# Kernel optimization log

Hardware: AMD Instinct MI355X
Metric: run time of the kernel (lower is better)

Reference implementation:

```python
import jax, jax.numpy as jnp
import numpy as np
from jax import lax


def setup_inputs() -> dict:
    key = jax.random.key(0)
    k1, k2, k3, k4 = jax.random.split(key, 4)
    N, D, B, R, EF = 100000, 256, 64, 32, 32
    storage = jax.random.normal(k1, (N, D), dtype=jnp.float32)
    query = jax.random.normal(k2, (B, D), dtype=jnp.float32)
    graph = jax.random.randint(k3, (N, R), 0, N, dtype=jnp.int32)      # fixed-degree NSW adjacency
    initial = jax.random.randint(k4, (B, EF), 0, N, dtype=jnp.int32)   # random entry points (entry())
    return {"query": query, "storage": storage, "graph": graph,
            "initial": initial, "k": 10, "ef_search": EF}


def reference(query, storage, graph, initial, k, ef_search):
    """Batched greedy best-first NSW search (ef_search fixed expansion steps)."""
    N = storage.shape[0]
    INF = jnp.float32(1e30)

    def sqdist(q, ids):
        diff = storage[ids] - q            # [R, D] gather
        return jnp.sum(diff * diff, axis=-1)

    def search_one(q, init):
        cd = sqdist(q, init)                               # candidate distances [EF]
        visited = jnp.zeros((N,), jnp.bool_).at[init].set(True)
        expanded = jnp.zeros((N,), jnp.bool_)

        def step(state, _):
            cid, cd, visited, expanded = state
            # pick closest unexpanded candidate
            pickd = jnp.where(expanded[cid], INF, cd)
            j = jnp.argmin(pickd)
            u = cid[j]
            expanded = expanded.at[u].set(True)
            # expand neighbors of u
            nbrs = graph[u]                                # [R]
            fresh = ~visited[nbrs]
            nd = jnp.where(fresh, sqdist(q, nbrs), INF)    # skip already-visited
            visited = visited.at[nbrs].set(True)
            # merge candidate pool, keep ef_search best
            all_ids = jnp.concatenate([cid, nbrs])
            all_d = jnp.concatenate([cd, nd])
            negd, idx = lax.top_k(-all_d, ef_search)
            return (all_ids[idx], -negd, visited, expanded), None

        (cid, cd, _, _), _ = lax.scan(step, (init, cd, visited, expanded),
                                      None, length=ef_search)
        negk, idx = lax.top_k(-cd, k)
        return cid[idx], -negk

    topk_ids, topk_dists = jax.vmap(search_one)(query, initial)
    return topk_ids, topk_dists
```

## Files before the change

### kernel.cpp

```cpp
#include <hip/hip_runtime.h>


#define DIMS   256
#define RDEG   32
#define EFPOOL 32
#define KOUT   10
#define NWORDS 3125
#define INF_D  1e30f

typedef unsigned long long u64;

__global__ __launch_bounds__(64, 1) void nsw_wave_kernel(
    const float* __restrict__ query,
    const float* __restrict__ storage,
    const int*   __restrict__ graph,
    const int*   __restrict__ initial,
    float*       __restrict__ out,
    int B)
{
    __shared__ unsigned int visited[NWORDS];
    __shared__ unsigned int expanded[NWORDS];
    __shared__ float4 qsh[DIMS / 4];
    __shared__ u64    keys[64];
    __shared__ float  sc_d[EFPOOL];
    __shared__ int    sc_id[EFPOOL];

    const int l    = threadIdx.x;
    const int b    = blockIdx.x;
    const int nb   = l & 31;
    const int half = l >> 5;

    for (int i = l; i < NWORDS; i += 64) { visited[i] = 0u; expanded[i] = 0u; }

    qsh[l] = reinterpret_cast<const float4*>(query + (size_t)b * DIMS)[l];

    float pool_d  = INF_D;
    int   pool_id = 0;
    int   u       = 0;
    int   nbid    = initial[b * EFPOOL + nb];

    for (int s = 0; s <= EFPOOL; ++s) {
        const bool is_init = (s == 0);

        if (!is_init && l == 0) expanded[u >> 5] |= 1u << (u & 31);

        unsigned vw = visited[nbid >> 5];
        bool fresh = is_init ? true : !((vw >> (nbid & 31)) & 1u);
        if ((l < 32) && fresh) atomicOr(&visited[nbid >> 5], 1u << (nbid & 31));

        float part = 0.f;
        if (fresh) {
            const float4* sp = reinterpret_cast<const float4*>(
                storage + (size_t)nbid * DIMS) + half * 32;
            float4 r[32];
            #pragma unroll
            for (int j = 0; j < 32; ++j) r[j] = sp[j];
            float a0 = 0.f, a1 = 0.f, a2 = 0.f, a3 = 0.f;
            #pragma unroll
            for (int j = 0; j < 32; ++j) {
                float4 q = qsh[half * 32 + j];
                float d0 = r[j].x - q.x; a0 = fmaf(d0, d0, a0);
                float d1 = r[j].y - q.y; a1 = fmaf(d1, d1, a1);
                float d2 = r[j].z - q.z; a2 = fmaf(d2, d2, a2);
                float d3 = r[j].w - q.w; a3 = fmaf(d3, d3, a3);
            }
            part = (a0 + a1) + (a2 + a3);
        }
        float d  = part + __shfl_xor(part, 32, 64);
        float nd = fresh ? d : INF_D;

        int nnbid = nbid;
        int uspec = -1;
        if (s < EFPOOL) {
            bool eflag = half ? (!fresh)
                              : (((expanded[pool_id >> 5] >> (pool_id & 31)) & 1u) != 0u);
            float ed_e = half ? nd : pool_d;
            unsigned ek = ((eflag ? 1u : 0u) << 31)
                        | ((__float_as_uint(ed_e) >> 13) << 6) | (unsigned)l;
            #pragma unroll
            for (int m = 1; m < 64; m <<= 1) {
                unsigned o = __shfl_xor((int)ek, m, 64);
                ek = (o < ek) ? o : ek;
            }
            int cidx  = (int)(ek & 63);
            int myid  = half ? nbid : pool_id;
            uspec = __shfl(myid, cidx, 64);
            nnbid = graph[(size_t)uspec * RDEG + nb];
        }

        {
            float ed  = half ? nd   : pool_d;
            int   eid = half ? nbid : pool_id;
            u64 key = ((u64)__float_as_uint(ed) << 6) | (unsigned)l;
            keys[l] = key;
            int rank = 0;
            #pragma unroll
            for (int j = 0; j < 64; ++j)
                rank += (keys[j] < key) ? 1 : 0;
            if (rank < EFPOOL) { sc_d[rank] = ed; sc_id[rank] = eid; }
            pool_d  = sc_d[nb];
            pool_id = sc_id[nb];
        }

        if (s < EFPOOL) {
            bool unexp = !((expanded[pool_id >> 5] >> (pool_id & 31)) & 1u);
            u64 bm = __ballot(unexp && (l < 32));
            int slot = (bm == 0ull) ? 0 : (__ffsll(bm) - 1);
            int utrue = sc_id[slot];
            int ut = __builtin_amdgcn_readfirstlane(utrue);
            int us = __builtin_amdgcn_readfirstlane(uspec);
            if (ut != us) {
                nnbid = graph[(size_t)ut * RDEG + nb];
            }
            u = utrue;
        }
        nbid = nnbid;
    }

    if (l < KOUT) {
        out[b * KOUT + l]            = (float)pool_id;
        out[B * KOUT + b * KOUT + l] = pool_d;
    }
}

extern "C" void kernel_launch(void* const* d_in, const int* in_sizes, int n_in,
                              void* d_out, int out_size, void* d_ws, size_t ws_size,
                              hipStream_t stream) {
    const float* query   = (const float*)d_in[0];
    const float* storage = (const float*)d_in[1];
    const int*   graph   = (const int*)d_in[2];
    const int*   initial = (const int*)d_in[3];
    float* out = (float*)d_out;

    const int B = in_sizes[0] / DIMS;

    nsw_wave_kernel<<<B, 64, 0, stream>>>(query, storage, graph, initial, out, B);
}
```

Baseline: 243.1 us.

## Prefetch next neighbor vectors at end of step and compute exact speculative pick

```diff
diff --git a/kernel.cpp b/kernel.cpp
--- a/kernel.cpp
+++ b/kernel.cpp
@@ -39,52 +39,60 @@
     int   u       = 0;
     int   nbid    = initial[b * EFPOOL + nb];
 
+    if (l < 32) atomicOr(&visited[nbid >> 5], 1u << (nbid & 31));
+
+    float4 r[32];
+    {
+        const float4* sp = reinterpret_cast<const float4*>(
+            storage + (size_t)nbid * DIMS) + half * 32;
+        #pragma unroll
+        for (int j = 0; j < 32; ++j) r[j] = sp[j];
+    }
+
     for (int s = 0; s <= EFPOOL; ++s) {
-        const bool is_init = (s == 0);
+        if (s > 0 && l == 0) expanded[u >> 5] |= 1u << (u & 31);
 
-        if (!is_init && l == 0) expanded[u >> 5] |= 1u << (u & 31);
+        bool fresh = true;
+        if (s > 0) {
+            unsigned vw = visited[nbid >> 5];
+            fresh = !((vw >> (nbid & 31)) & 1u);
+            if ((l < 32) && fresh) atomicOr(&visited[nbid >> 5], 1u << (nbid & 31));
+        }
 
-        unsigned vw = visited[nbid >> 5];
-        bool fresh = is_init ? true : !((vw >> (nbid & 31)) & 1u);
-        if ((l < 32) && fresh) atomicOr(&visited[nbid >> 5], 1u << (nbid & 31));
+        bool ounexp = !((expanded[pool_id >> 5] >> (pool_id & 31)) & 1u);
+        u64  obm    = __ballot(ounexp && (l < 32));
+        int  oslot  = (obm == 0ull) ? 0 : (__ffsll(obm) - 1);
+        float old_d = __shfl(pool_d,  oslot, 64);
+        int   old_id= __shfl(pool_id, oslot, 64);
+        bool  old_ok= (obm != 0ull);
 
-        float part = 0.f;
-        if (fresh) {
-            const float4* sp = reinterpret_cast<const float4*>(
-                storage + (size_t)nbid * DIMS) + half * 32;
-            float4 r[32];
-            #pragma unroll
-            for (int j = 0; j < 32; ++j) r[j] = sp[j];
-            float a0 = 0.f, a1 = 0.f, a2 = 0.f, a3 = 0.f;
-            #pragma unroll
-            for (int j = 0; j < 32; ++j) {
-                float4 q = qsh[half * 32 + j];
-                float d0 = r[j].x - q.x; a0 = fmaf(d0, d0, a0);
-                float d1 = r[j].y - q.y; a1 = fmaf(d1, d1, a1);
-                float d2 = r[j].z - q.z; a2 = fmaf(d2, d2, a2);
-                float d3 = r[j].w - q.w; a3 = fmaf(d3, d3, a3);
-            }
-            part = (a0 + a1) + (a2 + a3);
+        float a0 = 0.f, a1 = 0.f, a2 = 0.f, a3 = 0.f;
+        #pragma unroll
+        for (int j = 0; j < 32; ++j) {
+            float4 q = qsh[half * 32 + j];
+            float d0 = r[j].x - q.x; a0 = fmaf(d0, d0, a0);
+            float d1 = r[j].y - q.y; a1 = fmaf(d1, d1, a1);
+            float d2 = r[j].z - q.z; a2 = fmaf(d2, d2, a2);
+            float d3 = r[j].w - q.w; a3 = fmaf(d3, d3, a3);
         }
+        float part = (a0 + a1) + (a2 + a3);
         float d  = part + __shfl_xor(part, 32, 64);
         float nd = fresh ? d : INF_D;
 
         int nnbid = nbid;
-        int uspec = -1;
+        int uspec = 0;
         if (s < EFPOOL) {
-            bool eflag = half ? (!fresh)
-                              : (((expanded[pool_id >> 5] >> (pool_id & 31)) & 1u) != 0u);
-            float ed_e = half ? nd : pool_d;
-            unsigned ek = ((eflag ? 1u : 0u) << 31)
-                        | ((__float_as_uint(ed_e) >> 13) << 6) | (unsigned)l;
+            u64 nk = fresh ? (((u64)__float_as_uint(nd) << 6) | (u64)(32 + nb))
+                           : ~0ull;
             #pragma unroll
             for (int m = 1; m < 64; m <<= 1) {
-                unsigned o = __shfl_xor((int)ek, m, 64);
-                ek = (o < ek) ? o : ek;
+                u64 o = __shfl_xor(nk, m, 64);
+                nk = (o < nk) ? o : nk;
             }
-            int cidx  = (int)(ek & 63);
-            int myid  = half ? nbid : pool_id;
-            uspec = __shfl(myid, cidx, 64);
+            int new_id = __shfl(nbid, ((int)(nk & 63) - 32) & 31, 64);
+            u64 ok = old_ok ? (((u64)__float_as_uint(old_d) << 6) | (u64)oslot)
+                            : ~0ull;
+            uspec = (ok < nk) ? old_id : new_id;
             nnbid = graph[(size_t)uspec * RDEG + nb];
         }
 
@@ -109,12 +117,15 @@
             int utrue = sc_id[slot];
             int ut = __builtin_amdgcn_readfirstlane(utrue);
             int us = __builtin_amdgcn_readfirstlane(uspec);
-            if (ut != us) {
-                nnbid = graph[(size_t)ut * RDEG + nb];
-            }
-            u = utrue;
+            if (ut != us)
+                nnbid = graph[(size_t)utrue * RDEG + nb];
+            u    = utrue;
+            nbid = nnbid;
+            const float4* sp = reinterpret_cast<const float4*>(
+                storage + (size_t)nbid * DIMS) + half * 32;
+            #pragma unroll
+            for (int j = 0; j < 32; ++j) r[j] = sp[j];
         }
-        nbid = nnbid;
     }
 
     if (l < KOUT) {
```

New measurement: 228.2 us. 1.07x faster.
